# Kernel optimization log

Measured on AMD Instinct MI355X. Metric: run time of the kernel, lower is better.

Reference implementation:

```python
import jax, jax.numpy as jnp
import numpy as np

N_HEADS = 16  # cfg.n_heads
ROPE_BASE = 10000.0


def _rope_sin_cos(T, head_dim, dtype):
    # standard NeoX-style rotary tables, shape (T, head_dim)
    inv_freq = 1.0 / (ROPE_BASE ** (jnp.arange(0, head_dim, 2, dtype=jnp.float32) / head_dim))
    freqs = jnp.arange(T, dtype=jnp.float32)[:, None] * inv_freq[None, :]  # (T, hd/2)
    emb = jnp.concatenate([freqs, freqs], axis=-1)                          # (T, hd)
    return jnp.sin(emb).astype(dtype), jnp.cos(emb).astype(dtype)


def _rotate_half(x):
    x1, x2 = jnp.split(x, 2, axis=-1)
    return jnp.concatenate([-x2, x1], axis=-1)


def setup_inputs() -> dict:
    key = jax.random.key(0)
    kx, kq, kp, kl = jax.random.split(key, 4)
    B, T, D = 4, 2048, 2048
    x = jax.random.normal(kx, (B, T, D), dtype=jnp.float32)
    # torch Linear weights: (out_features, in_features), no bias
    Wqkv = jax.random.normal(kq, (3 * D, D), dtype=jnp.float32) * (D ** -0.5)
    Wproj = jax.random.normal(kp, (D, D), dtype=jnp.float32) * (D ** -0.5)
    # padding at the end: valid lengths in [T//2, T]
    lengths = jax.random.randint(kl, (B,), T // 2, T + 1)
    attention_mask = (jnp.arange(T)[None, :] < lengths[:, None]).astype(jnp.int32)
    return {"x": x, "Wqkv": Wqkv, "Wproj": Wproj, "attention_mask": attention_mask}


def reference(x, Wqkv, Wproj, attention_mask):
    B, T, D = x.shape
    H = N_HEADS
    hd = D // H
    qkv = (x @ Wqkv.T).reshape(B, T, 3, H, hd)            # (B,T,3,H,hd)
    q, k, v = (jnp.moveaxis(qkv[:, :, i], 1, 2) for i in range(3))  # each (B,H,T,hd)
    sin, cos = _rope_sin_cos(T, hd, x.dtype)              # (T,hd), broadcast over B,H
    q = q * cos + _rotate_half(q) * sin
    k = k * cos + _rotate_half(k) * sin
    scale = 1.0 / jnp.sqrt(jnp.asarray(hd, x.dtype))
    scores = jnp.einsum("bhqd,bhkd->bhqk", q, k) * scale  # (B,H,T,T)
    causal = jnp.triu(jnp.ones((T, T), dtype=bool), k=1)[None, None]       # (1,1,T,T)
    pad = (attention_mask == 0)[:, None, None, :]                           # (B,1,1,T)
    bias = jnp.where(causal | pad, -jnp.inf, 0.0).astype(x.dtype)
    attn = jax.nn.softmax(scores + bias, axis=-1)
    out = jnp.einsum("bhqk,bhkd->bhqd", attn, v)          # (B,H,T,hd)
    out = jnp.moveaxis(out, 1, 2).reshape(B, T, D)
    return out @ Wproj.T
```

## Files before the change

### kernel.cpp

```cpp
#include <hip/hip_runtime.h>
#include <math.h>

#define B_SZ 4
#define T_SEQ 2048
#define D_MODEL 2048
#define NH 16
#define HD 128

typedef unsigned short u16;
typedef unsigned int u32;
typedef __attribute__((ext_vector_type(8))) short short8;
typedef __attribute__((ext_vector_type(4))) float f32x4;

__device__ __forceinline__ float bf2f(u16 u) {
    return __uint_as_float(((u32)u) << 16);
}
__device__ __forceinline__ u16 f2bf(float f) {
    u32 x = __float_as_uint(f);
    return (u16)((x + 0x7fffu + ((x >> 16) & 1u)) >> 16);
}

__device__ __forceinline__ void gload_lds16(const u16* g, u16* lds) {
    __builtin_amdgcn_global_load_lds(
        (const __attribute__((address_space(1))) u32*)(const void*)g,
        (__attribute__((address_space(3))) u32*)(void*)lds, 16, 0, 0);
}

__global__ __launch_bounds__(256) void cast_kernel(const float* __restrict__ in,
                                                   u16* __restrict__ out, int n4)
{
    int idx = blockIdx.x * 256 + threadIdx.x;
    if (idx < n4) {
        float4 x = ((const float4*)in)[idx];
        ushort4 u;
        u.x = f2bf(x.x); u.y = f2bf(x.y); u.z = f2bf(x.z); u.w = f2bf(x.w);
        ((ushort4*)out)[idx] = u;
    }
}

#define TSZ 16384
#define MFMA_B16 __builtin_amdgcn_mfma_f32_16x16x32_bf16

template <int MODE>
__global__ __launch_bounds__(512, 2) void gemm256(
    const u16* __restrict__ A, const u16* __restrict__ W,
    float* __restrict__ C,
    u16* __restrict__ qb, u16* __restrict__ kb, u16* __restrict__ vb,
    int M, int N, int K)
{
    extern __shared__ u16 smem[];

    const int tid = threadIdx.x;
    const int nbx = N >> 8;
    const int nwg = gridDim.x;
    const int orig = blockIdx.x;
    const int wgid = (orig & 7) * (nwg >> 3) + (orig >> 3);
    const int bx = wgid % nbx, by = wgid / nbx;
    const int n0 = bx << 8, m0 = by << 8;

    const int w = tid >> 6, L = tid & 63;
    const int wm = w >> 2, wn = w & 3;
    const int lr = L & 15;
    const int lqb = (L >> 4) << 4;
    const int xorv = (lr & 7) << 4;
    const int cb0 = lqb ^ xorv;
    const int cb1 = (64 + lqb) ^ xorv;

    const u16* Ag = A + (size_t)m0 * K;
    const u16* Wg = W + (size_t)n0 * K;

    const int srow = tid >> 3;
    const int scb = ((tid << 4) & 127) ^ ((srow & 7) << 4);
    const size_t goff = (size_t)srow * K + (scb >> 1);
    const int loff = tid << 3;

    const int NT = K >> 6;

    f32x4 acc[8][4];
#pragma unroll
    for (int i = 0; i < 8; ++i)
#pragma unroll
        for (int j = 0; j < 4; ++j) acc[i][j] = (f32x4){0.f, 0.f, 0.f, 0.f};

#define ST_A(tt, c) gload_lds16(Ag + (size_t)((c) * 64) * K + (size_t)(tt) * 64 + goff, \
                                smem + ((tt) & 1) * TSZ + (c) * 4096 + loff)
#define ST_B(tt, c) gload_lds16(Wg + (size_t)((c) * 64) * K + (size_t)(tt) * 64 + goff, \
                                smem + 2 * TSZ + ((tt) & 1) * TSZ + (c) * 4096 + loff)

    ST_A(0, 0); ST_A(0, 2); ST_B(0, 0); ST_B(0, 1); ST_B(0, 2); ST_B(0, 3);
    ST_A(0, 1); ST_A(0, 3);
    ST_A(1, 0); ST_A(1, 2); ST_B(1, 0); ST_B(1, 1); ST_B(1, 2); ST_B(1, 3);
    asm volatile("s_waitcnt vmcnt(6)" ::: "memory");
    __builtin_amdgcn_s_barrier();

    for (int t = 0; t < NT; ++t) {
        const char* pA = (const char*)(smem + (t & 1) * TSZ) + (wm * 128 + lr) * 128;
        const char* pB = (const char*)(smem + 2 * TSZ + (t & 1) * TSZ) + (wn * 64 + lr) * 128;
        short8 alo[4][2], ahi[4][2], blo[2][2], bhi[2][2];

#pragma unroll
        for (int f = 0; f < 4; ++f) {
            alo[f][0] = *(const short8*)(pA + f * 2048 + cb0);
            alo[f][1] = *(const short8*)(pA + f * 2048 + cb1);
        }
#pragma unroll
        for (int g = 0; g < 2; ++g) {
            blo[g][0] = *(const short8*)(pB + g * 2048 + cb0);
            blo[g][1] = *(const short8*)(pB + g * 2048 + cb1);
        }
        if (t + 1 < NT) { ST_A(t + 1, 1); ST_A(t + 1, 3); }
        asm volatile("s_waitcnt lgkmcnt(8)" ::: "memory");
        __builtin_amdgcn_s_barrier();
        asm volatile("s_waitcnt lgkmcnt(0)" ::: "memory");
        __builtin_amdgcn_sched_barrier(0);
        __builtin_amdgcn_s_setprio(1);
#pragma unroll
        for (int f = 0; f < 4; ++f)
#pragma unroll
            for (int g = 0; g < 2; ++g) {
                acc[f][g] = MFMA_B16(alo[f][0], blo[g][0], acc[f][g], 0, 0, 0);
                acc[f][g] = MFMA_B16(alo[f][1], blo[g][1], acc[f][g], 0, 0, 0);
            }
        __builtin_amdgcn_s_setprio(0);
        __builtin_amdgcn_s_barrier();

#pragma unroll
        for (int g = 0; g < 2; ++g) {
            bhi[g][0] = *(const short8*)(pB + 4096 + g * 2048 + cb0);
            bhi[g][1] = *(const short8*)(pB + 4096 + g * 2048 + cb1);
        }
        if (t + 2 < NT) { ST_A(t + 2, 0); ST_A(t + 2, 2); }
        __builtin_amdgcn_s_barrier();
        asm volatile("s_waitcnt lgkmcnt(0)" ::: "memory");
        __builtin_amdgcn_sched_barrier(0);
        __builtin_amdgcn_s_setprio(1);
#pragma unroll
        for (int f = 0; f < 4; ++f)
#pragma unroll
            for (int g = 0; g < 2; ++g) {
                acc[f][2 + g] = MFMA_B16(alo[f][0], bhi[g][0], acc[f][2 + g], 0, 0, 0);
                acc[f][2 + g] = MFMA_B16(alo[f][1], bhi[g][1], acc[f][2 + g], 0, 0, 0);
            }
        __builtin_amdgcn_s_setprio(0);
        __builtin_amdgcn_s_barrier();

#pragma unroll
        for (int f = 0; f < 4; ++f) {
            ahi[f][0] = *(const short8*)(pA + 8192 + f * 2048 + cb0);
            ahi[f][1] = *(const short8*)(pA + 8192 + f * 2048 + cb1);
        }
        if (t + 2 < NT) { ST_B(t + 2, 0); ST_B(t + 2, 1); }
        __builtin_amdgcn_s_barrier();
        asm volatile("s_waitcnt lgkmcnt(0)" ::: "memory");
        __builtin_amdgcn_sched_barrier(0);
        __builtin_amdgcn_s_setprio(1);
#pragma unroll
        for (int f = 0; f < 4; ++f)
#pragma unroll
            for (int g = 0; g < 2; ++g) {
                acc[4 + f][g] = MFMA_B16(ahi[f][0], blo[g][0], acc[4 + f][g], 0, 0, 0);
                acc[4 + f][g] = MFMA_B16(ahi[f][1], blo[g][1], acc[4 + f][g], 0, 0, 0);
            }
        __builtin_amdgcn_s_setprio(0);
        __builtin_amdgcn_s_barrier();

        if (t + 2 < NT) { ST_B(t + 2, 2); ST_B(t + 2, 3); }
        if (t < NT - 2)
            asm volatile("s_waitcnt vmcnt(6)" ::: "memory");
        else
            asm volatile("s_waitcnt vmcnt(0)" ::: "memory");
        __builtin_amdgcn_s_barrier();
        __builtin_amdgcn_s_setprio(1);
#pragma unroll
        for (int f = 0; f < 4; ++f)
#pragma unroll
            for (int g = 0; g < 2; ++g) {
                acc[4 + f][2 + g] = MFMA_B16(ahi[f][0], bhi[g][0], acc[4 + f][2 + g], 0, 0, 0);
                acc[4 + f][2 + g] = MFMA_B16(ahi[f][1], bhi[g][1], acc[4 + f][2 + g], 0, 0, 0);
            }
        __builtin_amdgcn_s_setprio(0);
        __builtin_amdgcn_s_barrier();
    }
#undef ST_A
#undef ST_B

    const int lq4 = (L >> 4) << 2;

    if (MODE == 0) {
#pragma unroll
        for (int f = 0; f < 8; ++f) {
            const int m = m0 + wm * 128 + (f >> 2) * 64 + (f & 3) * 16 + lq4;
#pragma unroll
            for (int g = 0; g < 4; ++g) {
                const int n = n0 + wn * 64 + (g >> 1) * 32 + (g & 1) * 16 + lr;
#pragma unroll
                for (int r = 0; r < 4; ++r)
                    C[(size_t)(m + r) * N + n] = acc[f][g][r];
            }
        }
    } else {
        const int s = n0 >> 11;
        const int b_ = m0 >> 11;
        const int t0 = m0 & (T_SEQ - 1);
        if (s == 2) {
            u16* Ts = smem;
#pragma unroll
            for (int f = 0; f < 8; ++f) {
                const int tl = wm * 128 + (f >> 2) * 64 + (f & 3) * 16 + lq4;
#pragma unroll
                for (int g = 0; g < 4; ++g) {
                    const int c = wn * 64 + (g >> 1) * 32 + (g & 1) * 16 + lr;
                    char* rowp = (char*)Ts + c * 512;
#pragma unroll
                    for (int r = 0; r < 4; ++r)
                        *(u16*)(rowp + (((tl + r) * 2) ^ ((c & 7) << 4))) =
                            f2bf(acc[f][g][r]);
                }
            }
            __syncthreads();
            const int h0 = (n0 & 2047) >> 7;
            const int tcb = (tid & 31) << 4;
#pragma unroll
            for (int pass = 0; pass < 16; ++pass) {
                const int c = pass * 16 + (tid >> 5);
                short8 vv = *(const short8*)((const char*)Ts + c * 512 +
                                             (tcb ^ ((c & 7) << 4)));
                const int hh = c >> 7, d = c & 127;
                *(short8*)(vb + ((size_t)(b_ * NH + h0 + hh) * HD + d) * T_SEQ +
                           t0 + (tcb >> 1)) = vv;
            }
        } else {
            u16* p = (s == 0) ? qb : kb;
            const int nb = n0 & 2047;
#pragma unroll
            for (int f = 0; f < 8; ++f) {
                const int tl = t0 + wm * 128 + (f >> 2) * 64 + (f & 3) * 16 + lq4;
#pragma unroll
                for (int g = 0; g < 4; ++g) {
                    const int nn = nb + wn * 64 + (g >> 1) * 32 + (g & 1) * 16 + lr;
                    const int hh = nn >> 7, d = nn & 127;
                    u16* pb = p + ((size_t)(b_ * NH + hh) * T_SEQ + tl) * HD + d;
#pragma unroll
                    for (int r = 0; r < 4; ++r)
                        pb[(size_t)r * HD] = f2bf(acc[f][g][r]);
                }
            }
        }
    }
}

__global__ __launch_bounds__(128) void rope_kernel(u16* __restrict__ qb,
                                                   u16* __restrict__ kb)
{
    const int bht = blockIdx.x;
    const int t = bht & (T_SEQ - 1);
    const int bh = bht >> 11;
    const int tid = threadIdx.x;
    const int i = tid & 63;
    u16* buf = (tid < 64) ? qb : kb;
    const size_t base = ((size_t)bh * T_SEQ + t) * HD;

    const float inv = expf(-(2.f * (float)i / 128.f) * 9.210340371976184f);
    const float ang = (float)t * inv;
    const float s = sinf(ang);
    const float c = cosf(ang);

    const float x1 = bf2f(buf[base + i]);
    const float x2 = bf2f(buf[base + i + 64]);
    buf[base + i]      = f2bf(x1 * c - x2 * s);
    buf[base + i + 64] = f2bf(x2 * c + x1 * s);
}

__device__ __forceinline__ void stage_k_512(const u16* g, u16* lds, int tid) {
#pragma unroll
    for (int c = 0; c < 2; ++c) {
        const int row = c * 32 + (tid >> 4);
        const int cb = ((tid & 15) * 16) ^ ((row & 7) << 4);
        gload_lds16(g + (size_t)row * HD + (cb >> 1), lds + c * 4096 + tid * 8);
    }
}
__device__ __forceinline__ void stage_v_512(const u16* g, u16* lds, int tid) {
#pragma unroll
    for (int c = 0; c < 2; ++c) {
        const int row = c * 64 + (tid >> 3);
        const int cb = ((tid & 7) * 16) ^ ((row & 7) << 4);
        gload_lds16(g + (size_t)row * T_SEQ + (cb >> 1), lds + c * 4096 + tid * 8);
    }
}

__global__ __launch_bounds__(512, 2) void attn_kernel(
    const u16* __restrict__ q, const u16* __restrict__ k,
    const u16* __restrict__ v, const int* __restrict__ mask,
    u16* __restrict__ o)
{
    extern __shared__ u16 smem[];
    u16* Kb = smem;
    u16* Vb = smem + 16384;

    const int tid = threadIdx.x;
    const int id = blockIdx.x;
    const int bh = id & 63;
    const int qi = 15 - (id >> 6);
    const int b = bh >> 4;
    const int q0 = qi * 128;
    const int w = tid >> 6, L = tid & 63;
    const int lr = L & 15;
    const int lqB = (L >> 4) * 16;
    const int xk = (lr & 7) << 4;
    const float scale = 0.08838834764831845f;
    const float NEG = -1e30f;

    char* PsW = (char*)smem + 65536 + w * 2048;

    const u16* qg = q + (size_t)bh * T_SEQ * HD;
    const u16* kg = k + (size_t)bh * T_SEQ * HD;
    const u16* vg = v + (size_t)bh * HD * T_SEQ;
    const int* mrow = mask + b * T_SEQ;

#pragma unroll
    for (int c = 0; c < 4; ++c) {
        const int row = c * 32 + (tid >> 4);
        const int cb = ((tid & 15) * 16) ^ ((row & 7) << 4);
        gload_lds16(qg + (size_t)(q0 + row) * HD + (cb >> 1),
                    smem + c * 4096 + tid * 8);
    }
    int4 m4 = ((const int4*)mrow)[tid];
    int part = m4.x + m4.y + m4.z + m4.w;
#pragma unroll
    for (int off = 32; off >= 1; off >>= 1) part += __shfl_xor(part, off);
    int* lred = (int*)((char*)smem + 65536);
    if (L == 0) lred[w] = part;
    __syncthreads();
    int len = 0;
#pragma unroll
    for (int i = 0; i < 8; ++i) len += lred[i];

    short8 qa[4];
    {
        const char* Qc = (const char*)smem;
        const int row = w * 16 + lr;
#pragma unroll
        for (int kc = 0; kc < 4; ++kc)
            qa[kc] = *(const short8*)(Qc + row * 256 + ((kc * 64 + lqB) ^ xk));
    }
    __syncthreads();

    const int lim = 2 * qi + 1;

    stage_k_512(kg, Kb, tid);
    stage_v_512(vg, Vb, tid);

    f32x4 on[8];
#pragma unroll
    for (int nd = 0; nd < 8; ++nd) on[nd] = (f32x4){0.f, 0.f, 0.f, 0.f};
    float l_r[4] = {0.f, 0.f, 0.f, 0.f};
    const int wrow0 = q0 + w * 16;
    const int row_base = wrow0 + (L >> 4) * 4;

    for (int kt = 0; kt <= lim; ++kt) {
        const int kv0 = kt * 64;
        const int cur = kt & 1;
        if (kt < lim) {
            stage_k_512(kg + (size_t)(kv0 + 64) * HD, Kb + (cur ^ 1) * 8192, tid);
            stage_v_512(vg + (kv0 + 64), Vb + (cur ^ 1) * 8192, tid);
            asm volatile("s_waitcnt vmcnt(4)" ::: "memory");
        } else {
            asm volatile("s_waitcnt vmcnt(0)" ::: "memory");
        }
        __builtin_amdgcn_s_barrier();

        const bool active = (kv0 <= wrow0 + 15);
        if (active) {
            const char* Kc = (const char*)(Kb + cur * 8192);
            const char* Vc = (const char*)(Vb + cur * 8192);

            f32x4 sacc[4];
#pragma unroll
            for (int nt = 0; nt < 4; ++nt) {
                const char* rp = Kc + (nt * 16 + lr) * 256;
                short8 bb[4];
#pragma unroll
                for (int kc = 0; kc < 4; ++kc)
                    bb[kc] = *(const short8*)(rp + ((kc * 64 + lqB) ^ xk));
                sacc[nt] = (f32x4){0.f, 0.f, 0.f, 0.f};
                __builtin_amdgcn_s_setprio(1);
#pragma unroll
                for (int kc = 0; kc < 4; ++kc)
                    sacc[nt] = MFMA_B16(qa[kc], bb[kc], sacc[nt], 0, 0, 0);
                __builtin_amdgcn_s_setprio(0);
            }

            const bool diag = (kv0 + 63 > wrow0);
#pragma unroll
            for (int nt = 0; nt < 4; ++nt) {
                const int col = kv0 + nt * 16 + lr;
                const float bias = (col < len) ? 0.f : NEG;
#pragma unroll
                for (int r = 0; r < 4; ++r) {
                    float s = sacc[nt][r] * scale + bias;
                    if (diag && col > row_base + r) s = NEG;
                    const float p = __expf(s);
                    l_r[r] += p;
                    const int pr = (L >> 4) * 4 + r;
                    *(u16*)(PsW + pr * 128 +
                            (((nt * 16 + lr) * 2) ^ ((pr & 7) << 4))) = f2bf(p);
                }
            }

            short8 pa0 = *(const short8*)(PsW + lr * 128 + (lqB ^ xk));
            short8 pa1 = *(const short8*)(PsW + lr * 128 + ((64 + lqB) ^ xk));
            __builtin_amdgcn_s_setprio(1);
#pragma unroll
            for (int nd = 0; nd < 8; ++nd) {
                const char* vp = Vc + (nd * 16 + lr) * 128;
                short8 vb0 = *(const short8*)(vp + (lqB ^ xk));
                short8 vb1 = *(const short8*)(vp + ((64 + lqB) ^ xk));
                on[nd] = MFMA_B16(pa0, vb0, on[nd], 0, 0, 0);
                on[nd] = MFMA_B16(pa1, vb1, on[nd], 0, 0, 0);
            }
            __builtin_amdgcn_s_setprio(0);
        }
        __builtin_amdgcn_s_barrier();
    }

#pragma unroll
    for (int off = 1; off < 16; off <<= 1)
#pragma unroll
        for (int r = 0; r < 4; ++r)
            l_r[r] += __shfl_xor(l_r[r], off);

    const int h = bh & 15;
#pragma unroll
    for (int r = 0; r < 4; ++r) {
        const float inv = 1.f / l_r[r];
        const int t = row_base + r;
        u16* op = o + ((size_t)(b * T_SEQ + t)) * D_MODEL + h * HD + lr;
#pragma unroll
        for (int nd = 0; nd < 8; ++nd)
            op[nd * 16] = f2bf(on[nd][r] * inv);
    }
}

extern "C" void kernel_launch(void* const* d_in, const int* in_sizes, int n_in,
                              void* d_out, int out_size, void* d_ws, size_t ws_size,
                              hipStream_t stream)
{
    const float* x     = (const float*)d_in[0];
    const float* Wqkv  = (const float*)d_in[1];
    const float* Wproj = (const float*)d_in[2];
    const int*   mask  = (const int*)d_in[3];
    float* out = (float*)d_out;

    const size_t E = (size_t)B_SZ * T_SEQ * D_MODEL;
    u16* xb     = (u16*)d_ws;
    u16* wqkvb  = xb + E;
    u16* wprojb = wqkvb + (size_t)3 * D_MODEL * D_MODEL;
    u16* qb     = wprojb + (size_t)D_MODEL * D_MODEL;
    u16* kb     = qb + E;
    u16* vb     = kb + E;
    u16* ob     = vb + E;

    const int M = B_SZ * T_SEQ;

    cast_kernel<<<dim3((int)(E / 4 / 256)), 256, 0, stream>>>(x, xb, (int)(E / 4));
    cast_kernel<<<dim3(3 * D_MODEL * D_MODEL / 4 / 256), 256, 0, stream>>>(
        Wqkv, wqkvb, 3 * D_MODEL * D_MODEL / 4);
    cast_kernel<<<dim3(D_MODEL * D_MODEL / 4 / 256), 256, 0, stream>>>(
        Wproj, wprojb, D_MODEL * D_MODEL / 4);

    gemm256<1><<<dim3((3 * D_MODEL / 256) * (M / 256)), 512, 131072, stream>>>(
        xb, wqkvb, nullptr, qb, kb, vb, M, 3 * D_MODEL, D_MODEL);

    rope_kernel<<<dim3(B_SZ * NH * T_SEQ), 128, 0, stream>>>(qb, kb);

    attn_kernel<<<dim3(16 * 64), 512, 81920, stream>>>(qb, kb, vb, mask, ob);

    gemm256<0><<<dim3((D_MODEL / 256) * (M / 256)), 512, 131072, stream>>>(
        ob, wprojb, out, nullptr, nullptr, nullptr, M, D_MODEL, D_MODEL);
}
```

Before: 578.1 us.

## Fuse RoPE into QKV GEMM epilogue via LDS staging and precomputed sin/cos table

Removes the standalone rope kernel by applying rotary embedding in the QKV GEMM epilogue. Q/K tiles are first staged in swizzled LDS so each thread can pair element d with d+64, then written out as 16-byte vectors. A small kernel precomputes a sin/cos table into the ob workspace, which attention overwrites later. Attention blocks are also remapped so each XCD handles a fixed set of heads for better L2 locality. The cost is an extra LDS round trip and barrier in the GEMM epilogue.

Result: slower. 596.2 us (+3.1%).

```diff
diff --git a/kernel.cpp b/kernel.cpp
--- a/kernel.cpp
+++ b/kernel.cpp
@@ -38,6 +38,16 @@
     }
 }
 
+__global__ __launch_bounds__(256) void rope_table_kernel(float* __restrict__ tab)
+{
+    const int idx = blockIdx.x * 256 + threadIdx.x;
+    const int t = idx >> 6, i = idx & 63;
+    const float inv = expf(-(2.f * (float)i / 128.f) * 9.210340371976184f);
+    const float ang = (float)t * inv;
+    tab[idx] = sinf(ang);
+    tab[131072 + idx] = cosf(ang);
+}
+
 #define TSZ 16384
 #define MFMA_B16 __builtin_amdgcn_mfma_f32_16x16x32_bf16
 
@@ -46,6 +56,7 @@
     const u16* __restrict__ A, const u16* __restrict__ W,
     float* __restrict__ C,
     u16* __restrict__ qb, u16* __restrict__ kb, u16* __restrict__ vb,
+    const float* __restrict__ ropetab,
     int M, int N, int K)
 {
     extern __shared__ u16 smem[];
@@ -202,6 +213,7 @@
         const int s = n0 >> 11;
         const int b_ = m0 >> 11;
         const int t0 = m0 & (T_SEQ - 1);
+        const int h0 = (n0 & 2047) >> 7;
         if (s == 2) {
             u16* Ts = smem;
 #pragma unroll
@@ -218,7 +230,6 @@
                 }
             }
             __syncthreads();
-            const int h0 = (n0 & 2047) >> 7;
             const int tcb = (tid & 31) << 4;
 #pragma unroll
             for (int pass = 0; pass < 16; ++pass) {
@@ -230,45 +241,59 @@
                            t0 + (tcb >> 1)) = vv;
             }
         } else {
+            u16* Ts = smem;
+#pragma unroll
+            for (int f = 0; f < 8; ++f) {
+                const int tl = wm * 128 + (f >> 2) * 64 + (f & 3) * 16 + lq4;
+#pragma unroll
+                for (int g = 0; g < 4; ++g) {
+                    const int nn = wn * 64 + (g >> 1) * 32 + (g & 1) * 16 + lr;
+#pragma unroll
+                    for (int r = 0; r < 4; ++r) {
+                        const int row = tl + r;
+                        *(u16*)((char*)Ts + row * 512 +
+                                ((nn * 2) ^ ((row & 7) << 4))) =
+                            f2bf(acc[f][g][r]);
+                    }
+                }
+            }
+            __syncthreads();
             u16* p = (s == 0) ? qb : kb;
-            const int nb = n0 & 2047;
-#pragma unroll
-            for (int f = 0; f < 8; ++f) {
-                const int tl = t0 + wm * 128 + (f >> 2) * 64 + (f & 3) * 16 + lq4;
-#pragma unroll
-                for (int g = 0; g < 4; ++g) {
-                    const int nn = nb + wn * 64 + (g >> 1) * 32 + (g & 1) * 16 + lr;
-                    const int hh = nn >> 7, d = nn & 127;
-                    u16* pb = p + ((size_t)(b_ * NH + hh) * T_SEQ + tl) * HD + d;
-#pragma unroll
-                    for (int r = 0; r < 4; ++r)
-                        pb[(size_t)r * HD] = f2bf(acc[f][g][r]);
+            const float* st = ropetab;
+            const float* ct = ropetab + 131072;
+#pragma unroll
+            for (int pass = 0; pass < 8; ++pass) {
+                const int task = pass * 512 + tid;
+                const int d0c = task & 7;
+                const int th = task >> 3;
+                const int tlr = th & 255;
+                const int head = th >> 8;
+                const int tg = t0 + tlr;
+                const char* rowp = (const char*)Ts + tlr * 512;
+                const int sw = (tlr & 7) << 4;
+                short8 lo = *(const short8*)(rowp + (((head * 256 + d0c * 16)) ^ sw));
+                short8 hi = *(const short8*)(rowp + (((head * 256 + 128 + d0c * 16)) ^ sw));
+                float4 s0 = *(const float4*)(st + tg * 64 + d0c * 8);
+                float4 s1 = *(const float4*)(st + tg * 64 + d0c * 8 + 4);
+                float4 c0 = *(const float4*)(ct + tg * 64 + d0c * 8);
+                float4 c1 = *(const float4*)(ct + tg * 64 + d0c * 8 + 4);
+                const float sv[8] = {s0.x, s0.y, s0.z, s0.w, s1.x, s1.y, s1.z, s1.w};
+                const float cv[8] = {c0.x, c0.y, c0.z, c0.w, c1.x, c1.y, c1.z, c1.w};
+                short8 olo, ohi;
+#pragma unroll
+                for (int e = 0; e < 8; ++e) {
+                    const float x1 = bf2f((u16)lo[e]);
+                    const float x2 = bf2f((u16)hi[e]);
+                    olo[e] = (short)f2bf(x1 * cv[e] - x2 * sv[e]);
+                    ohi[e] = (short)f2bf(x2 * cv[e] + x1 * sv[e]);
                 }
-            }
-        }
-    }
-}
-
-__global__ __launch_bounds__(128) void rope_kernel(u16* __restrict__ qb,
-                                                   u16* __restrict__ kb)
-{
-    const int bht = blockIdx.x;
-    const int t = bht & (T_SEQ - 1);
-    const int bh = bht >> 11;
-    const int tid = threadIdx.x;
-    const int i = tid & 63;
-    u16* buf = (tid < 64) ? qb : kb;
-    const size_t base = ((size_t)bh * T_SEQ + t) * HD;
-
-    const float inv = expf(-(2.f * (float)i / 128.f) * 9.210340371976184f);
-    const float ang = (float)t * inv;
-    const float s = sinf(ang);
-    const float c = cosf(ang);
-
-    const float x1 = bf2f(buf[base + i]);
-    const float x2 = bf2f(buf[base + i + 64]);
-    buf[base + i]      = f2bf(x1 * c - x2 * s);
-    buf[base + i + 64] = f2bf(x2 * c + x1 * s);
+                u16* pb = p + ((size_t)(b_ * NH + h0 + head) * T_SEQ + tg) * HD +
+                          d0c * 8;
+                *(short8*)(pb) = olo;
+                *(short8*)(pb + 64) = ohi;
+            }
+        }
+    }
 }
 
 __device__ __forceinline__ void stage_k_512(const u16* g, u16* lds, int tid) {
@@ -298,9 +323,11 @@
     u16* Vb = smem + 16384;
 
     const int tid = threadIdx.x;
-    const int id = blockIdx.x;
-    const int bh = id & 63;
-    const int qi = 15 - (id >> 6);
+    const int orig = blockIdx.x;
+    const int xcd = orig & 7;
+    const int slot = orig >> 3;
+    const int bh = xcd + ((slot >> 4) << 3);
+    const int qi = 15 - (slot & 15);
     const int b = bh >> 4;
     const int q0 = qi * 128;
     const int w = tid >> 6, L = tid & 63;
@@ -459,6 +486,7 @@
     u16* kb     = qb + E;
     u16* vb     = kb + E;
     u16* ob     = vb + E;
+    float* ropetab = (float*)ob;
 
     const int M = B_SZ * T_SEQ;
 
@@ -467,14 +495,13 @@
         Wqkv, wqkvb, 3 * D_MODEL * D_MODEL / 4);
     cast_kernel<<<dim3(D_MODEL * D_MODEL / 4 / 256), 256, 0, stream>>>(
         Wproj, wprojb, D_MODEL * D_MODEL / 4);
+    rope_table_kernel<<<dim3(512), 256, 0, stream>>>(ropetab);
 
     gemm256<1><<<dim3((3 * D_MODEL / 256) * (M / 256)), 512, 131072, stream>>>(
-        xb, wqkvb, nullptr, qb, kb, vb, M, 3 * D_MODEL, D_MODEL);
-
-    rope_kernel<<<dim3(B_SZ * NH * T_SEQ), 128, 0, stream>>>(qb, kb);
+        xb, wqkvb, nullptr, qb, kb, vb, ropetab, M, 3 * D_MODEL, D_MODEL);
 
     attn_kernel<<<dim3(16 * 64), 512, 81920, stream>>>(qb, kb, vb, mask, ob);
 
     gemm256<0><<<dim3((D_MODEL / 256) * (M / 256)), 512, 131072, stream>>>(
-        ob, wprojb, out, nullptr, nullptr, nullptr, M, D_MODEL, D_MODEL);
-}
+        ob, wprojb, out, nullptr, nullptr, nullptr, nullptr, M, D_MODEL, D_MODEL);
+}
```
